# Kernel optimization log

Measured on AMD Instinct MI355X. Metric: run time of the kernel, lower is better.

## Reference

```python
import jax, jax.numpy as jnp
import numpy as np

B, N, C = 16, 1024, 768
D = 512
DEPTH = 4
K = 3
HP = WP = 32
A_EPS = 1e-4
POW_MIN = 1e-20
LN_EPS = 1e-5


def setup_inputs() -> dict:
    key = jax.random.key(0)
    ks = jax.random.split(key, 20)
    inp = {
        "tokens": jax.random.normal(ks[0], (B, N, C), dtype=jnp.float32),
        "in_proj_w": jax.random.normal(ks[1], (C, D), dtype=jnp.float32) * 0.02,
        "in_proj_b": jnp.zeros((D,), dtype=jnp.float32),
        "blk_norm_w": jnp.ones((DEPTH, D), dtype=jnp.float32),
        "blk_norm_b": jnp.zeros((DEPTH, D), dtype=jnp.float32),
        "blk_inp_w": jax.random.normal(ks[2], (DEPTH, D, 2 * D), dtype=jnp.float32) * 0.02,
        "blk_inp_b": jnp.zeros((DEPTH, 2 * D), dtype=jnp.float32),
        "blk_conv_w": jax.random.normal(ks[3], (DEPTH, K, K, 1, D), dtype=jnp.float32) * 0.1,
        "blk_conv_b": jnp.zeros((DEPTH, D), dtype=jnp.float32),
        "blk_a_logit": jax.random.normal(ks[4], (DEPTH, D), dtype=jnp.float32) * 0.1,
        "blk_b": jnp.ones((DEPTH, D), dtype=jnp.float32) + jax.random.normal(ks[5], (DEPTH, D), dtype=jnp.float32) * 0.02,
        "blk_c": jnp.ones((DEPTH, D), dtype=jnp.float32) + jax.random.normal(ks[6], (DEPTH, D), dtype=jnp.float32) * 0.02,
        "blk_d": jnp.ones((DEPTH, D), dtype=jnp.float32) + jax.random.normal(ks[7], (DEPTH, D), dtype=jnp.float32) * 0.02,
        "blk_out_w": jax.random.normal(ks[8], (DEPTH, D, D), dtype=jnp.float32) * 0.02,
        "blk_out_b": jnp.zeros((DEPTH, D), dtype=jnp.float32),
        "out_norm_w": jnp.ones((D,), dtype=jnp.float32),
        "out_norm_b": jnp.zeros((D,), dtype=jnp.float32),
    }
    return inp


def _layernorm(x, w, b):
    mu = jnp.mean(x, axis=-1, keepdims=True)
    var = jnp.var(x, axis=-1, keepdims=True)
    return (x - mu) * jax.lax.rsqrt(var + LN_EPS) * w + b


def _ssm_scan(x, a_logit, bb, cc, dd):
    # x: (B', L, D)   s_t = a s_{t-1} + b x_t ; y_t = c s_t + d x_t  (log-domain cumsum form)
    L = x.shape[1]
    a = jnp.clip(jax.nn.sigmoid(a_logit), A_EPS, 1.0 - A_EPS)
    t = jnp.arange(L, dtype=jnp.float32)
    a_pow = jnp.maximum(jnp.exp(t[:, None] * jnp.log(a)[None, :]), POW_MIN)  # (L, D)
    u = x * bb  # (B', L, D)
    r = jnp.cumsum(u / a_pow[None], axis=1)
    s = r * a_pow[None]
    return s * cc + x * dd


def _scan2d(x, a_logit, bb, cc, dd):
    # x: (B, H, W, D); bidirectional row-major + col-major scans, averaged
    Bb, H, W, Dd = x.shape
    L = H * W
    seq_row = x.reshape(Bb, L, Dd)
    seq_col = jnp.transpose(x, (0, 2, 1, 3)).reshape(Bb, L, Dd)
    seqs = jnp.concatenate([seq_row, seq_col], axis=0)            # (2B, L, D)
    all_seqs = jnp.concatenate([seqs, seqs[:, ::-1]], axis=0)     # (4B, L, D)
    y2 = _ssm_scan(all_seqs, a_logit, bb, cc, dd)
    y_f, y_rev = jnp.split(y2, 2, axis=0)
    y = 0.5 * (y_f + y_rev[:, ::-1])
    y_row, y_col = jnp.split(y, 2, axis=0)
    y_row_map = y_row.reshape(Bb, H, W, Dd)
    y_col_map = jnp.transpose(y_col.reshape(Bb, W, H, Dd), (0, 2, 1, 3))
    return 0.5 * (y_row_map + y_col_map)


def _dwconv_silu(x, kernel, bias):
    # x: (B,H,W,D); kernel: (K,K,1,D) depthwise; SAME padding (odd k)
    y = jax.lax.conv_general_dilated(
        x, kernel, window_strides=(1, 1), padding="SAME",
        feature_group_count=x.shape[-1],
        dimension_numbers=("NHWC", "HWIO", "NHWC"))
    return jax.nn.silu(y + bias)


def _block(x, nw, nb, iw, ib, cw, cb, al, sb, sc, sd, ow, ob):
    h = _layernorm(x, nw, nb)
    xg = h @ iw + ib                      # (B,H,W,2D)
    x_in, gate = jnp.split(xg, 2, axis=-1)
    gate = jax.nn.sigmoid(gate)
    u = _dwconv_silu(x_in, cw, cb)
    y = _scan2d(u, al, sb, sc, sd)
    y = (y * gate) @ ow + ob
    return x + y


def reference(tokens, in_proj_w, in_proj_b, blk_norm_w, blk_norm_b, blk_inp_w,
              blk_inp_b, blk_conv_w, blk_conv_b, blk_a_logit, blk_b, blk_c,
              blk_d, blk_out_w, blk_out_b, out_norm_w, out_norm_b):
    x = tokens @ in_proj_w + in_proj_b          # (B, N, D)
    x = x.reshape(B, HP, WP, D)                 # token grid
    for i in range(DEPTH):
        x = _block(x, blk_norm_w[i], blk_norm_b[i], blk_inp_w[i], blk_inp_b[i],
                   blk_conv_w[i], blk_conv_b[i], blk_a_logit[i], blk_b[i],
                   blk_c[i], blk_d[i], blk_out_w[i], blk_out_b[i])
    x = _layernorm(x, out_norm_w, out_norm_b)
    return jnp.mean(x, axis=(1, 2))             # pooled global vector (B, D)
```

## Files before the change

kernel.cpp:

```cpp
#include <hip/hip_runtime.h>
#include <hip/hip_bf16.h>
#include <math.h>

#define NPOS 16384
#define DD   512
#define PP   ((size_t)NPOS * DD)

typedef __bf16 bf16x8 __attribute__((ext_vector_type(8)));
typedef float  f32x4  __attribute__((ext_vector_type(4)));

__device__ __forceinline__ void gload16(const __bf16* g, __bf16* l) {
  __builtin_amdgcn_global_load_lds((__attribute__((address_space(1))) void*)(g),
                                   (__attribute__((address_space(3))) void*)(l), 16, 0, 0);
}
__device__ __forceinline__ void wait_vm0() { asm volatile("s_waitcnt vmcnt(0)" ::: "memory"); }
__device__ __forceinline__ void wait_vm2() { asm volatile("s_waitcnt vmcnt(2)" ::: "memory"); }
__device__ __forceinline__ void wait_vm3() { asm volatile("s_waitcnt vmcnt(3)" ::: "memory"); }
__device__ __forceinline__ void wait_lgkm0() { asm volatile("s_waitcnt lgkmcnt(0)" ::: "memory"); }

template<int BDIR>
__global__ __launch_bounds__(512, 4) void gemm_k(
    const __bf16* __restrict__ A, const __bf16* __restrict__ Bt,
    const float* __restrict__ bias, const float* __restrict__ res,
    float* __restrict__ C0, __bf16* __restrict__ C1, __bf16* __restrict__ C1b,
    int N, int K, int epi)
{
  __shared__ __bf16 SM[BDIR ? 20480 : 24576];
  __bf16 (*Asm)[4096] = (__bf16(*)[4096])SM;
  __bf16 (*Bsm)[4096] = (__bf16(*)[4096])(SM + 3 * 4096);

  const int tid  = threadIdx.x;
  const int w    = tid >> 6;
  const int lane = tid & 63;
  const int quad = lane >> 4;
  const int l16  = lane & 15;
  const int wm   = (w >> 2) << 6;
  const int wn   = (w & 3) << 5;

  const int nwg = gridDim.x;
  const int cpx = nwg >> 3;
  const int lin = (blockIdx.x & 7) * cpx + (blockIdx.x >> 3);
  const int nbn = N >> 7;
  const int sh  = (nbn == 8) ? 3 : 2;
  const int mt  = lin >> sh;
  const int ntc = lin & (nbn - 1);
  const int bm  = mt << 7;
  const int bn  = ntc << 7;

  const __bf16* Ab = A + (size_t)bm * K;
  const __bf16* Bb = Bt + (size_t)bn * K;
  const __bf16* Bp0 = Bt + (size_t)(bn + wn + l16) * K + quad * 8;
  const __bf16* Bp1 = Bp0 + (size_t)16 * K;
  const int nk = K >> 5;

  f32x4 acc[4][2];
  #pragma unroll
  for (int i = 0; i < 4; ++i)
    #pragma unroll
    for (int j = 0; j < 2; ++j) acc[i][j] = (f32x4){0.f, 0.f, 0.f, 0.f};

  #define STG(P, gb, tile, buf) {                                               \
    const int r_ = tid >> 2, c_ = tid & 3;                                      \
    gload16(gb + (size_t)r_ * K + ((tile) << 5) + ((c_ ^ ((r_ >> 1) & 3)) << 3),\
            &P[buf][tid << 3]);                                                 \
  }

  int cur = 0;
  if constexpr (BDIR == 0) {
    STG(Asm, Ab, 0, 0) STG(Bsm, Bb, 0, 0)
    STG(Asm, Ab, 1, 1) STG(Bsm, Bb, 1, 1)
    wait_vm2();
    __builtin_amdgcn_s_barrier();

    for (int t = 0; t < nk; ++t) {
      const int nx2 = (cur == 0) ? 2 : cur - 1;
      const bool st = (t + 2 < nk);
      if (st) {
        STG(Asm, Ab, t + 2, nx2)
        STG(Bsm, Bb, t + 2, nx2)
      }
      bf16x8 af[4], bfr[2];
      #pragma unroll
      for (int i = 0; i < 4; ++i) {
        const int m = wm + i * 16 + l16;
        af[i] = *(const bf16x8*)(&Asm[cur][m * 32 + ((quad ^ ((m >> 1) & 3)) << 3)]);
      }
      #pragma unroll
      for (int j = 0; j < 2; ++j) {
        const int n = wn + j * 16 + l16;
        bfr[j] = *(const bf16x8*)(&Bsm[cur][n * 32 + ((quad ^ ((n >> 1) & 3)) << 3)]);
      }
      __builtin_amdgcn_s_setprio(1);
      #pragma unroll
      for (int i = 0; i < 4; ++i) {
        acc[i][0] = __builtin_amdgcn_mfma_f32_16x16x32_bf16(af[i], bfr[0], acc[i][0], 0, 0, 0);
        acc[i][1] = __builtin_amdgcn_mfma_f32_16x16x32_bf16(af[i], bfr[1], acc[i][1], 0, 0, 0);
      }
      __builtin_amdgcn_s_setprio(0);
      if (st) { wait_vm2(); } else { wait_vm0(); }
      __builtin_amdgcn_s_barrier();
      cur = (cur == 2) ? 0 : cur + 1;
    }
  } else {
    STG(Asm, Ab, 0, 0)
    STG(Asm, Ab, 1, 1)
    bf16x8 bq0 = *(const bf16x8*)(Bp0);
    bf16x8 bq1 = *(const bf16x8*)(Bp1);
    bf16x8 br0 = *(const bf16x8*)(Bp0 + 32);
    bf16x8 br1 = *(const bf16x8*)(Bp1 + 32);
    wait_vm0();
    __builtin_amdgcn_s_barrier();

    for (int t = 0; t < nk; ++t) {
      const int nx2 = (cur == 0) ? 2 : cur - 1;
      const bool st = (t + 2 < nk);
      bf16x8 bs0 = br0, bs1 = br1;
      if (st) {
        STG(Asm, Ab, t + 2, nx2)
        bs0 = *(const bf16x8*)(Bp0 + ((t + 2) << 5));
        bs1 = *(const bf16x8*)(Bp1 + ((t + 2) << 5));
      }
      bf16x8 af[4];
      #pragma unroll
      for (int i = 0; i < 4; ++i) {
        const int m = wm + i * 16 + l16;
        af[i] = *(const bf16x8*)(&Asm[cur][m * 32 + ((quad ^ ((m >> 1) & 3)) << 3)]);
      }
      __builtin_amdgcn_s_setprio(1);
      #pragma unroll
      for (int i = 0; i < 4; ++i) {
        acc[i][0] = __builtin_amdgcn_mfma_f32_16x16x32_bf16(af[i], bq0, acc[i][0], 0, 0, 0);
        acc[i][1] = __builtin_amdgcn_mfma_f32_16x16x32_bf16(af[i], bq1, acc[i][1], 0, 0, 0);
      }
      __builtin_amdgcn_s_setprio(0);
      if (st) { wait_vm3(); } else if (t + 1 < nk) { wait_vm0(); }
      __builtin_amdgcn_s_barrier();
      bq0 = br0; bq1 = br1; br0 = bs0; br1 = bs1;
      cur = (cur == 2) ? 0 : cur + 1;
    }
  }
  #undef STG

  if (epi == 1) {
    const bool dosig = (bn >= 512);
    __bf16* dst = dosig ? C1 : C1b;
    const int cb = dosig ? (bn - 512) : bn;
    char* wb = (char*)SM + w * 5120;
    #pragma unroll
    for (int i = 0; i < 4; ++i)
      #pragma unroll
      for (int j = 0; j < 2; ++j) {
        const float bv = bias[bn + wn + j * 16 + l16];
        #pragma unroll
        for (int r = 0; r < 4; ++r) {
          float v = acc[i][j][r] + bv;
          if (dosig) v = 1.f / (1.f + expf(-v));
          *(__bf16*)(wb + (i * 16 + quad * 4 + r) * 80 + (j * 16 + l16) * 2) = (__bf16)v;
        }
      }
    wait_lgkm0();
    #pragma unroll
    for (int s = 0; s < 4; ++s) {
      const int rr = s * 16 + (lane >> 2);
      bf16x8 vv = *(bf16x8*)(wb + rr * 80 + (lane & 3) * 16);
      const int grow = bm + wm + rr;
      *(bf16x8*)(dst + (size_t)grow * 512 + cb + wn + (lane & 3) * 8) = vv;
    }
  } else {
    #pragma unroll
    for (int j = 0; j < 2; ++j) {
      const int col = wn + j * 16 + l16;
      const float bv = bias[bn + col];
      #pragma unroll
      for (int i = 0; i < 4; ++i) {
        const int row0 = bm + wm + i * 16 + quad * 4;
        #pragma unroll
        for (int r = 0; r < 4; ++r) {
          float v = acc[i][j][r] + bv;
          size_t off = (size_t)(row0 + r) * N + bn + col;
          if (epi == 2) v += res[off];
          C0[off] = v;
        }
      }
    }
  }
}

__global__ __launch_bounds__(256) void cvt_k(const float* __restrict__ s, __bf16* __restrict__ d)
{
  size_t i = ((size_t)blockIdx.x * 256 + threadIdx.x) * 8;
  float4 a = *(const float4*)(s + i);
  float4 b = *(const float4*)(s + i + 4);
  bf16x8 v;
  v[0] = (__bf16)a.x; v[1] = (__bf16)a.y; v[2] = (__bf16)a.z; v[3] = (__bf16)a.w;
  v[4] = (__bf16)b.x; v[5] = (__bf16)b.y; v[6] = (__bf16)b.z; v[7] = (__bf16)b.w;
  *(bf16x8*)(d + i) = v;
}

__global__ __launch_bounds__(256) void tr_k(const float* __restrict__ src, __bf16* __restrict__ dst,
                                            int K, int N, size_t sstr, size_t dstr)
{
  __shared__ float t[32][33];
  const float* s = src + blockIdx.z * sstr;
  __bf16* d = dst + blockIdx.z * dstr;
  int n0 = blockIdx.x * 32, k0 = blockIdx.y * 32;
  int tx = threadIdx.x & 31, ty = threadIdx.x >> 5;
  #pragma unroll
  for (int i = 0; i < 4; ++i)
    t[ty + i * 8][tx] = s[(size_t)(k0 + ty + i * 8) * N + n0 + tx];
  __syncthreads();
  #pragma unroll
  for (int i = 0; i < 4; ++i)
    d[(size_t)(n0 + ty + i * 8) * K + k0 + tx] = (__bf16)t[tx][ty + i * 8];
}

__global__ __launch_bounds__(256) void ln_k(const float* __restrict__ x, const float* __restrict__ w,
                                            const float* __restrict__ bv, __bf16* __restrict__ out)
{
  int gw = (blockIdx.x * 256 + threadIdx.x) >> 6;
  int lane = threadIdx.x & 63;
  const float* xp = x + ((size_t)gw << 9) + lane * 8;
  float4 u0 = *(const float4*)xp;
  float4 u1 = *(const float4*)(xp + 4);
  float v[8] = {u0.x,u0.y,u0.z,u0.w,u1.x,u1.y,u1.z,u1.w};
  float s = 0.f;
  #pragma unroll
  for (int j = 0; j < 8; ++j) s += v[j];
  #pragma unroll
  for (int off = 32; off; off >>= 1) s += __shfl_xor(s, off, 64);
  float mu = s * (1.f/512.f);
  float q = 0.f;
  #pragma unroll
  for (int j = 0; j < 8; ++j) { float d = v[j] - mu; q += d*d; }
  #pragma unroll
  for (int off = 32; off; off >>= 1) q += __shfl_xor(q, off, 64);
  float rstd = rsqrtf(q * (1.f/512.f) + 1e-5f);
  int dch = lane * 8;
  float4 w0 = *(const float4*)(w + dch),  w1 = *(const float4*)(w + dch + 4);
  float4 b0 = *(const float4*)(bv + dch), b1 = *(const float4*)(bv + dch + 4);
  float wv[8] = {w0.x,w0.y,w0.z,w0.w,w1.x,w1.y,w1.z,w1.w};
  float bb[8] = {b0.x,b0.y,b0.z,b0.w,b1.x,b1.y,b1.z,b1.w};
  bf16x8 ov;
  #pragma unroll
  for (int j = 0; j < 8; ++j) ov[j] = (__bf16)((v[j] - mu) * rstd * wv[j] + bb[j]);
  *(bf16x8*)(out + ((size_t)gw << 9) + dch) = ov;
}

__device__ __forceinline__ float sig_a(float al) {
  float a = 1.f / (1.f + expf(-al));
  return fminf(fmaxf(a, 1e-4f), 1.f - 1e-4f);
}

#define CST 544

__global__ __launch_bounds__(512, 4) void scan2d_k(
    const __bf16* __restrict__ xin, const float* __restrict__ cw, const float* __restrict__ cb,
    const float* __restrict__ alog, const float* __restrict__ bvec, const float* __restrict__ cvec,
    const float* __restrict__ dvec, const __bf16* __restrict__ gate, __bf16* __restrict__ yo)
{
  __shared__ __bf16 T[32 * CST];
  __shared__ __bf16 Y[32 * CST];
  __shared__ float  S[4][32][16];
  const int tid = threadIdx.x;
  const int bx  = blockIdx.x;
  const int cg  = ((bx & 7) << 2) | (bx >> 3);
  const int b   = blockIdx.y;
  const int ch  = tid & 15;
  const int c0  = tid >> 4;
  const int d   = (cg << 4) + ch;

  const float a   = sig_a(alog[d]);
  const float lna = logf(a);
  const float ia  = 1.f / a;
  const float bb  = bvec[d];
  const float sc  = 0.25f * cvec[d];
  const float dd  = dvec[d];

  const __bf16* ub = xin + ((size_t)b << 19) + (cg << 4);

  #pragma unroll
  for (int i = 0; i < 4; ++i) {
    int f = tid + i * 512;
    int pos = f >> 1, half = f & 1;
    *(bf16x8*)(T + (pos >> 5) * CST + ((pos & 31) << 4) + (half << 3))
        = *(const bf16x8*)(ub + (size_t)pos * 512 + (half << 3));
  }
  float w00 = cw[(0 << 9) + d], w01 = cw[(1 << 9) + d], w02 = cw[(2 << 9) + d];
  float w10 = cw[(3 << 9) + d], w11 = cw[(4 << 9) + d], w12 = cw[(5 << 9) + d];
  float w20 = cw[(6 << 9) + d], w21 = cw[(7 << 9) + d], w22 = cw[(8 << 9) + d];
  const float cbv = cb[d];
  const float A0f = expf((float)(c0 << 5) * lna),        R0f = expf((float)(c0 << 5) * -lna);
  const float A0b = expf((float)((31 - c0) << 5) * lna), R0b = expf((float)((31 - c0) << 5) * -lna);
  __syncthreads();

  {
    const bool up = (c0 > 0);
    const bool dn = (c0 < 31);
    float a0 = 0.f, a1 = 0.f, a2 = 0.f;
    float b0 = up ? (float)T[(c0 - 1) * CST + ch] : 0.f;
    float b1 =      (float)T[c0 * CST + ch];
    float b2 = dn ? (float)T[(c0 + 1) * CST + ch] : 0.f;
    #pragma unroll 4
    for (int ww = 0; ww < 32; ++ww) {
      float e0 = 0.f, e1 = 0.f, e2 = 0.f;
      if (ww < 31) {
        e0 = up ? (float)T[(c0 - 1) * CST + ((ww + 1) << 4) + ch] : 0.f;
        e1 =      (float)T[c0 * CST + ((ww + 1) << 4) + ch];
        e2 = dn ? (float)T[(c0 + 1) * CST + ((ww + 1) << 4) + ch] : 0.f;
      }
      float acc0 = cbv;
      acc0 = fmaf(a0, w00, acc0); acc0 = fmaf(b0, w01, acc0); acc0 = fmaf(e0, w02, acc0);
      acc0 = fmaf(a1, w10, acc0); acc0 = fmaf(b1, w11, acc0); acc0 = fmaf(e1, w12, acc0);
      acc0 = fmaf(a2, w20, acc0); acc0 = fmaf(b2, w21, acc0); acc0 = fmaf(e2, w22, acc0);
      acc0 = acc0 / (1.f + expf(-acc0));
      Y[c0 * CST + (ww << 4) + ch] = (__bf16)acc0;
      a0 = b0; a1 = b1; a2 = b2; b0 = e0; b1 = e1; b2 = e2;
    }
  }
  __syncthreads();

  #define STEP(r_, uu_, apr_, rp_)                                 \
    { float rr_ = (apr_ < 1e-20f) ? 1e20f : rp_;                   \
      r_ = fmaf((uu_) * bb, rr_, r_); }

  {
    float pf = A0f, qf = R0f, pb = A0b, qb = R0b;
    float s0 = 0.f, s1 = 0.f, s2 = 0.f, s3 = 0.f;
    #pragma unroll 4
    for (int j = 0; j < 32; ++j) {
      float urf = (float)Y[c0 * CST + (j << 4) + ch];
      float urb = (float)Y[c0 * CST + ((31 - j) << 4) + ch];
      float ucf = (float)Y[j * CST + (c0 << 4) + ch];
      float ucb = (float)Y[(31 - j) * CST + (c0 << 4) + ch];
      STEP(s0, urf, pf, qf)  STEP(s2, ucf, pf, qf)
      STEP(s1, urb, pb, qb)  STEP(s3, ucb, pb, qb)
      pf *= a; qf *= ia; pb *= a; qb *= ia;
    }
    S[0][c0][ch] = s0; S[1][c0][ch] = s1; S[2][c0][ch] = s2; S[3][c0][ch] = s3;
  }
  __syncthreads();

  if (tid < 64) {
    int arr = tid >> 4, ch2 = tid & 15;
    float run = 0.f;
    if ((arr & 1) == 0) {
      #pragma unroll 4
      for (int cc = 0; cc < 32; ++cc) { float v = S[arr][cc][ch2]; S[arr][cc][ch2] = run; run += v; }
    } else {
      #pragma unroll 4
      for (int cc = 31; cc >= 0; --cc) { float v = S[arr][cc][ch2]; S[arr][cc][ch2] = run; run += v; }
    }
  }
  __syncthreads();

  {
    float r = S[2][c0][ch];
    float p = A0f, q = R0f;
    #pragma unroll 4
    for (int j = 0; j < 32; ++j) {
      int i0 = j * CST + (c0 << 4) + ch;
      float u = (float)Y[i0];
      float ap = fmaxf(p, 1e-20f);
      STEP(r, u, p, q)
      T[i0] = (__bf16)(r * ap);
      p *= a; q *= ia;
    }
  }
  {
    float r = S[3][c0][ch];
    float p = A0b, q = R0b;
    #pragma unroll 4
    for (int j = 31; j >= 0; --j) {
      int i0 = j * CST + (c0 << 4) + ch;
      float u = (float)Y[i0];
      float ap = fmaxf(p, 1e-20f);
      STEP(r, u, p, q)
      T[i0] = (__bf16)(sc * ((float)T[i0] + r * ap));
      p *= a; q *= ia;
    }
  }
  __syncthreads();

  {
    float r = S[0][c0][ch];
    float p = A0f, q = R0f;
    #pragma unroll 4
    for (int j = 0; j < 32; ++j) {
      int i0 = c0 * CST + (j << 4) + ch;
      float u = (float)Y[i0];
      float ap = fmaxf(p, 1e-20f);
      STEP(r, u, p, q)
      T[i0] = (__bf16)((float)T[i0] + sc * (r * ap));
      p *= a; q *= ia;
    }
  }
  {
    const __bf16* gb = gate + ((size_t)b << 19) + (cg << 4) + ch;
    __bf16* yb = yo + ((size_t)b << 19) + (cg << 4) + ch;
    float r = S[1][c0][ch];
    float p = A0b, q = R0b;
    #pragma unroll 4
    for (int j = 31; j >= 0; --j) {
      int pp = (c0 << 5) + j;
      int i0 = c0 * CST + (j << 4) + ch;
      float u = (float)Y[i0];
      float ap = fmaxf(p, 1e-20f);
      STEP(r, u, p, q)
      float y0 = (float)T[i0] + sc * (r * ap) + dd * u;
      yb[(size_t)pp * 512] = (__bf16)(y0 * (float)gb[(size_t)pp * 512]);
      p *= a; q *= ia;
    }
  }
  #undef STEP
}

__global__ __launch_bounds__(256) void reduce_k(const __bf16* __restrict__ hn, float* __restrict__ out)
{
  __shared__ float part[4][64];
  int l = threadIdx.x & 63;
  int q = threadIdx.x >> 6;
  int d = blockIdx.y * 64 + l;
  int b = blockIdx.x;
  const __bf16* p = hn + ((size_t)b << 19) + d + ((size_t)(q * 256) << 9);
  float s0 = 0.f, s1 = 0.f, s2 = 0.f, s3 = 0.f;
  for (int t = 0; t < 256; t += 4) {
    s0 += (float)p[(size_t)(t+0) << 9];
    s1 += (float)p[(size_t)(t+1) << 9];
    s2 += (float)p[(size_t)(t+2) << 9];
    s3 += (float)p[(size_t)(t+3) << 9];
  }
  part[q][l] = (s0 + s1) + (s2 + s3);
  __syncthreads();
  if (threadIdx.x < 64)
    out[b * 512 + d] = (part[0][l] + part[1][l] + part[2][l] + part[3][l]) * (1.f / 1024.f);
}

extern "C" void kernel_launch(void* const* d_in, const int* in_sizes, int n_in,
                              void* d_out, int out_size, void* d_ws, size_t ws_size,
                              hipStream_t stream)
{
  const float* tokens = (const float*)d_in[0];
  const float* in_w   = (const float*)d_in[1];
  const float* in_b   = (const float*)d_in[2];
  const float* nw     = (const float*)d_in[3];
  const float* nb     = (const float*)d_in[4];
  const float* iw     = (const float*)d_in[5];
  const float* ib     = (const float*)d_in[6];
  const float* cw     = (const float*)d_in[7];
  const float* cb     = (const float*)d_in[8];
  const float* al     = (const float*)d_in[9];
  const float* bbv    = (const float*)d_in[10];
  const float* ccv    = (const float*)d_in[11];
  const float* ddv    = (const float*)d_in[12];
  const float* ow     = (const float*)d_in[13];
  const float* obv    = (const float*)d_in[14];
  const float* onw    = (const float*)d_in[15];
  const float* onb    = (const float*)d_in[16];

  float*  x     = (float*)d_ws;
  __bf16* hy16  = (__bf16*)(x + PP);
  __bf16* xin16 = hy16 + PP;
  __bf16* g16   = xin16 + PP;
  __bf16* iwT   = g16 + PP;
  __bf16* owT   = iwT + (size_t)4 * 1024 * 512;
  __bf16* tb16  = owT + (size_t)4 * 512 * 512;
  __bf16* inwT  = xin16;

  cvt_k<<<6144, 256, 0, stream>>>(tokens, tb16);
  tr_k<<<dim3(16, 24, 1), 256, 0, stream>>>(in_w, inwT, 768, 512, 0, 0);
  tr_k<<<dim3(32, 16, 4), 256, 0, stream>>>(iw, iwT, 512, 1024, (size_t)512*1024, (size_t)1024*512);
  tr_k<<<dim3(16, 16, 4), 256, 0, stream>>>(ow, owT, 512, 512, (size_t)512*512, (size_t)512*512);

  gemm_k<0><<<512, 512, 0, stream>>>(tb16, inwT, in_b, nullptr, x, nullptr, nullptr,
                                     512, 768, 0);

  for (int i = 0; i < 4; ++i) {
    ln_k<<<4096, 256, 0, stream>>>(x, nw + i*512, nb + i*512, hy16);
    gemm_k<1><<<1024, 512, 0, stream>>>(hy16, iwT + (size_t)i*1024*512, ib + i*1024,
                                        nullptr, nullptr, g16, xin16, 1024, 512, 1);
    scan2d_k<<<dim3(32, 16), 512, 0, stream>>>(xin16, cw + i*9*512, cb + i*512,
                                               al + i*512, bbv + i*512, ccv + i*512,
                                               ddv + i*512, g16, hy16);
    gemm_k<0><<<512, 512, 0, stream>>>(hy16, owT + (size_t)i*512*512, obv + i*512,
                                       x, x, nullptr, nullptr, 512, 512, 2);
  }

  ln_k<<<4096, 256, 0, stream>>>(x, onw, onb, hy16);
  reduce_k<<<dim3(16, 8), 256, 0, stream>>>(hy16, (float*)d_out);
}
```

Measured before the change: 598.7 us.

## Widen input-projection GEMM tile to 128x256 with LDS-staged B operand

The block input-projection GEMM now uses a 128x256 output tile per workgroup. Each wave computes a 64x64 sub-tile with 16 MFMAs per k-step, and the grid is halved. The B operand is staged through LDS with async global-to-LDS loads in a triple buffer, where it used to be streamed per-wave from global memory into registers. The aim is more operand reuse per loaded byte and fewer redundant global reads of the weights, at the cost of more LDS, more accumulator registers and a smaller grid, which may reduce occupancy and parallelism.

Measured after the change: 566.3 us. -5.4%, faster.

```diff
diff --git a/kernel.cpp b/kernel.cpp
--- a/kernel.cpp
+++ b/kernel.cpp
@@ -18,16 +18,17 @@
 __device__ __forceinline__ void wait_vm3() { asm volatile("s_waitcnt vmcnt(3)" ::: "memory"); }
 __device__ __forceinline__ void wait_lgkm0() { asm volatile("s_waitcnt lgkmcnt(0)" ::: "memory"); }
 
-template<int BDIR>
+template<int BN256>
 __global__ __launch_bounds__(512, 4) void gemm_k(
     const __bf16* __restrict__ A, const __bf16* __restrict__ Bt,
     const float* __restrict__ bias, const float* __restrict__ res,
     float* __restrict__ C0, __bf16* __restrict__ C1, __bf16* __restrict__ C1b,
     int N, int K, int epi)
 {
-  __shared__ __bf16 SM[BDIR ? 20480 : 24576];
-  __bf16 (*Asm)[4096] = (__bf16(*)[4096])SM;
-  __bf16 (*Bsm)[4096] = (__bf16(*)[4096])(SM + 3 * 4096);
+  __shared__ __bf16 SM[BN256 ? 36864 : 24576];
+  __bf16 (*Asm)[4096]  = (__bf16(*)[4096])SM;
+  __bf16 (*Bsm)[4096]  = (__bf16(*)[4096])(SM + 12288);
+  __bf16 (*BsmW)[8192] = (__bf16(*)[8192])(SM + 12288);
 
   const int tid  = threadIdx.x;
   const int w    = tid >> 6;
@@ -35,40 +36,50 @@
   const int quad = lane >> 4;
   const int l16  = lane & 15;
   const int wm   = (w >> 2) << 6;
-  const int wn   = (w & 3) << 5;
+  const int wn   = (w & 3) << (BN256 ? 6 : 5);
+  constexpr int JW = BN256 ? 4 : 2;
 
   const int nwg = gridDim.x;
   const int cpx = nwg >> 3;
   const int lin = (blockIdx.x & 7) * cpx + (blockIdx.x >> 3);
-  const int nbn = N >> 7;
-  const int sh  = (nbn == 8) ? 3 : 2;
+  const int nbn = BN256 ? (N >> 8) : (N >> 7);
+  const int sh  = (nbn == 8) ? 3 : ((nbn == 4) ? 2 : 1);
   const int mt  = lin >> sh;
   const int ntc = lin & (nbn - 1);
   const int bm  = mt << 7;
-  const int bn  = ntc << 7;
-
-  const __bf16* Ab = A + (size_t)bm * K;
+  const int bn  = ntc << (BN256 ? 8 : 7);
+
+  const __bf16* Ab = A  + (size_t)bm * K;
   const __bf16* Bb = Bt + (size_t)bn * K;
-  const __bf16* Bp0 = Bt + (size_t)(bn + wn + l16) * K + quad * 8;
-  const __bf16* Bp1 = Bp0 + (size_t)16 * K;
   const int nk = K >> 5;
 
-  f32x4 acc[4][2];
+  f32x4 acc[4][JW];
   #pragma unroll
   for (int i = 0; i < 4; ++i)
     #pragma unroll
-    for (int j = 0; j < 2; ++j) acc[i][j] = (f32x4){0.f, 0.f, 0.f, 0.f};
-
-  #define STG(P, gb, tile, buf) {                                               \
-    const int r_ = tid >> 2, c_ = tid & 3;                                      \
-    gload16(gb + (size_t)r_ * K + ((tile) << 5) + ((c_ ^ ((r_ >> 1) & 3)) << 3),\
-            &P[buf][tid << 3]);                                                 \
+    for (int j = 0; j < JW; ++j) acc[i][j] = (f32x4){0.f, 0.f, 0.f, 0.f};
+
+  #define STG_A(tile, buf) {                                                     \
+    const int r_ = tid >> 2, c_ = tid & 3;                                       \
+    gload16(Ab + (size_t)r_ * K + ((tile) << 5) + ((c_ ^ ((r_ >> 1) & 3)) << 3), \
+            &Asm[buf][tid << 3]);                                                \
+  }
+  #define STG_B(tile, buf) {                                                     \
+    const int r_ = tid >> 2, c_ = tid & 3;                                       \
+    gload16(Bb + (size_t)r_ * K + ((tile) << 5) + ((c_ ^ ((r_ >> 1) & 3)) << 3), \
+            &Bsm[buf][tid << 3]);                                                \
+  }
+  #define STG_B2(tile, buf, k2) {                                                \
+    const int ch_ = tid + ((k2) << 9);                                           \
+    const int r_ = ch_ >> 2, c_ = ch_ & 3;                                       \
+    gload16(Bb + (size_t)r_ * K + ((tile) << 5) + ((c_ ^ ((r_ >> 1) & 3)) << 3), \
+            &BsmW[buf][ch_ << 3]);                                               \
   }
 
   int cur = 0;
-  if constexpr (BDIR == 0) {
-    STG(Asm, Ab, 0, 0) STG(Bsm, Bb, 0, 0)
-    STG(Asm, Ab, 1, 1) STG(Bsm, Bb, 1, 1)
+  if constexpr (BN256 == 0) {
+    STG_A(0, 0) STG_B(0, 0)
+    STG_A(1, 1) STG_B(1, 1)
     wait_vm2();
     __builtin_amdgcn_s_barrier();
 
@@ -76,8 +87,8 @@
       const int nx2 = (cur == 0) ? 2 : cur - 1;
       const bool st = (t + 2 < nk);
       if (st) {
-        STG(Asm, Ab, t + 2, nx2)
-        STG(Bsm, Bb, t + 2, nx2)
+        STG_A(t + 2, nx2)
+        STG_B(t + 2, nx2)
       }
       bf16x8 af[4], bfr[2];
       #pragma unroll
@@ -102,70 +113,73 @@
       cur = (cur == 2) ? 0 : cur + 1;
     }
   } else {
-    STG(Asm, Ab, 0, 0)
-    STG(Asm, Ab, 1, 1)
-    bf16x8 bq0 = *(const bf16x8*)(Bp0);
-    bf16x8 bq1 = *(const bf16x8*)(Bp1);
-    bf16x8 br0 = *(const bf16x8*)(Bp0 + 32);
-    bf16x8 br1 = *(const bf16x8*)(Bp1 + 32);
-    wait_vm0();
+    STG_A(0, 0) STG_B2(0, 0, 0) STG_B2(0, 0, 1)
+    STG_A(1, 1) STG_B2(1, 1, 0) STG_B2(1, 1, 1)
+    wait_vm3();
     __builtin_amdgcn_s_barrier();
 
     for (int t = 0; t < nk; ++t) {
       const int nx2 = (cur == 0) ? 2 : cur - 1;
       const bool st = (t + 2 < nk);
-      bf16x8 bs0 = br0, bs1 = br1;
       if (st) {
-        STG(Asm, Ab, t + 2, nx2)
-        bs0 = *(const bf16x8*)(Bp0 + ((t + 2) << 5));
-        bs1 = *(const bf16x8*)(Bp1 + ((t + 2) << 5));
-      }
-      bf16x8 af[4];
+        STG_A(t + 2, nx2)
+        STG_B2(t + 2, nx2, 0)
+        STG_B2(t + 2, nx2, 1)
+      }
+      bf16x8 af[4], bfr[4];
       #pragma unroll
       for (int i = 0; i < 4; ++i) {
         const int m = wm + i * 16 + l16;
         af[i] = *(const bf16x8*)(&Asm[cur][m * 32 + ((quad ^ ((m >> 1) & 3)) << 3)]);
       }
+      #pragma unroll
+      for (int j = 0; j < 4; ++j) {
+        const int n = wn + j * 16 + l16;
+        bfr[j] = *(const bf16x8*)(&BsmW[cur][n * 32 + ((quad ^ ((n >> 1) & 3)) << 3)]);
+      }
       __builtin_amdgcn_s_setprio(1);
       #pragma unroll
-      for (int i = 0; i < 4; ++i) {
-        acc[i][0] = __builtin_amdgcn_mfma_f32_16x16x32_bf16(af[i], bq0, acc[i][0], 0, 0, 0);
-        acc[i][1] = __builtin_amdgcn_mfma_f32_16x16x32_bf16(af[i], bq1, acc[i][1], 0, 0, 0);
-      }
+      for (int i = 0; i < 4; ++i)
+        #pragma unroll
+        for (int j = 0; j < 4; ++j)
+          acc[i][j] = __builtin_amdgcn_mfma_f32_16x16x32_bf16(af[i], bfr[j], acc[i][j], 0, 0, 0);
       __builtin_amdgcn_s_setprio(0);
-      if (st) { wait_vm3(); } else if (t + 1 < nk) { wait_vm0(); }
+      if (st) { wait_vm3(); } else { wait_vm0(); }
       __builtin_amdgcn_s_barrier();
-      bq0 = br0; bq1 = br1; br0 = bs0; br1 = bs1;
       cur = (cur == 2) ? 0 : cur + 1;
     }
   }
-  #undef STG
-
-  if (epi == 1) {
+  #undef STG_A
+  #undef STG_B
+  #undef STG_B2
+
+  if constexpr (BN256) {
     const bool dosig = (bn >= 512);
     __bf16* dst = dosig ? C1 : C1b;
     const int cb = dosig ? (bn - 512) : bn;
-    char* wb = (char*)SM + w * 5120;
+    char* wb = (char*)SM + w * 9216;
     #pragma unroll
     for (int i = 0; i < 4; ++i)
       #pragma unroll
-      for (int j = 0; j < 2; ++j) {
+      for (int j = 0; j < 4; ++j) {
         const float bv = bias[bn + wn + j * 16 + l16];
         #pragma unroll
         for (int r = 0; r < 4; ++r) {
           float v = acc[i][j][r] + bv;
           if (dosig) v = 1.f / (1.f + expf(-v));
-          *(__bf16*)(wb + (i * 16 + quad * 4 + r) * 80 + (j * 16 + l16) * 2) = (__bf16)v;
+          *(__bf16*)(wb + (i * 16 + quad * 4 + r) * 144 + (j * 16 + l16) * 2) = (__bf16)v;
         }
       }
     wait_lgkm0();
     #pragma unroll
-    for (int s = 0; s < 4; ++s) {
-      const int rr = s * 16 + (lane >> 2);
-      bf16x8 vv = *(bf16x8*)(wb + rr * 80 + (lane & 3) * 16);
-      const int grow = bm + wm + rr;
-      *(bf16x8*)(dst + (size_t)grow * 512 + cb + wn + (lane & 3) * 8) = vv;
-    }
+    for (int i = 0; i < 4; ++i)
+      #pragma unroll
+      for (int h = 0; h < 2; ++h) {
+        const int rr = (lane >> 3) + h * 8;
+        bf16x8 vv = *(bf16x8*)(wb + (i * 16 + rr) * 144 + (lane & 7) * 16);
+        const int grow = bm + wm + i * 16 + rr;
+        *(bf16x8*)(dst + (size_t)grow * 512 + cb + wn + (lane & 7) * 8) = vv;
+      }
   } else {
     #pragma unroll
     for (int j = 0; j < 2; ++j) {
@@ -476,8 +490,8 @@
 
   for (int i = 0; i < 4; ++i) {
     ln_k<<<4096, 256, 0, stream>>>(x, nw + i*512, nb + i*512, hy16);
-    gemm_k<1><<<1024, 512, 0, stream>>>(hy16, iwT + (size_t)i*1024*512, ib + i*1024,
-                                        nullptr, nullptr, g16, xin16, 1024, 512, 1);
+    gemm_k<1><<<512, 512, 0, stream>>>(hy16, iwT + (size_t)i*1024*512, ib + i*1024,
+                                       nullptr, nullptr, g16, xin16, 1024, 512, 1);
     scan2d_k<<<dim3(32, 16), 512, 0, stream>>>(xin16, cw + i*9*512, cb + i*512,
                                                al + i*512, bbv + i*512, ccv + i*512,
                                                ddv + i*512, g16, hy16);
```
